# Kernel tuning notes

Measured on AMD Instinct MI355X. Metric: run time of the kernel, lower is better.

## Reference

```python
import jax, jax.numpy as jnp
import numpy as np

N = 50000      # nodes
E = 800000     # edges
IN = 256       # in_dim
D = 64         # hidden_dim per head
H = 4          # heads
OUT = 40       # out_dim (classes)
SLOPE = 0.2    # leaky relu negative slope


def _gat_conv(h, src, dst, W, al, ar, heads, dh, res=None, act=False):
    """DGL-style GATConv. h:[N,Fin], W:[Fin,heads*dh], al/ar:[heads,dh]."""
    n = h.shape[0]
    feat = (h @ W).reshape(n, heads, dh)                 # [N,H,D]
    el = jnp.sum(feat * al, axis=-1)                     # [N,H]
    er = jnp.sum(feat * ar, axis=-1)                     # [N,H]
    e = jax.nn.leaky_relu(el[src] + er[dst], SLOPE)      # [E,H]
    # segment softmax over incoming edges of each dst node
    m = jax.ops.segment_max(e, dst, num_segments=n)      # [N,H]
    ex = jnp.exp(e - m[dst])                             # [E,H]
    s = jax.ops.segment_sum(ex, dst, num_segments=n)     # [N,H]
    alpha = ex / s[dst]                                  # [E,H]
    rst = jax.ops.segment_sum(alpha[:, :, None] * feat[src], dst, num_segments=n)  # [N,H,D]
    if res is not None:
        rst = rst + res
    if act:
        rst = jax.nn.elu(rst)
    return rst


def setup_inputs():
    key = jax.random.key(0)
    ks = jax.random.split(key, 16)
    def p(k, shape, fan_in):
        return (jax.random.normal(k, shape, jnp.float32) / np.sqrt(fan_in)).astype(jnp.float32)
    inputs = jax.random.normal(ks[0], (N, IN), jnp.float32)
    src = jax.random.randint(ks[1], (E,), 0, N, dtype=jnp.int32)
    dst = jax.random.randint(ks[2], (E,), 0, N, dtype=jnp.int32)
    return {
        "inputs": inputs, "src": src, "dst": dst,
        "W0": p(ks[3], (IN, H * D), IN), "al0": p(ks[4], (H, D), D), "ar0": p(ks[5], (H, D), D),
        "W1": p(ks[6], (H * D, H * D), H * D), "al1": p(ks[7], (H, D), D), "ar1": p(ks[8], (H, D), D),
        "Wo": p(ks[9], (H * D, H * OUT), H * D), "alo": p(ks[10], (H, OUT), OUT), "aro": p(ks[11], (H, OUT), OUT),
        "res_Wo": p(ks[12], (H * D, H * OUT), H * D),
        "fc_W": p(ks[13], (IN, D), IN),
    }


def reference(inputs, src, dst, W0, al0, ar0, W1, al1, ar1, Wo, alo, aro, res_Wo, fc_W):
    # layer 0: no residual, elu activation
    h = _gat_conv(inputs, src, dst, W0, al0, ar0, H, D, res=None, act=True)
    h = h.reshape(N, H * D)
    # layer 1: identity residual (in_feats == heads*out_feats), elu
    res1 = h.reshape(N, H, D)
    h = _gat_conv(h, src, dst, W1, al1, ar1, H, D, res=res1, act=True)
    h = h.reshape(N, H * D)
    # output layer: linear residual projection, no activation, mean over heads
    res_o = (h @ res_Wo).reshape(N, H, OUT)
    logits = _gat_conv(h, src, dst, Wo, alo, aro, H, OUT, res=res_o, act=False).mean(axis=1)
    seq_fts = inputs @ fc_W
    return (logits, h, seq_fts)
```

## Files before the change

### kernel.cpp

```cpp
#include <hip/hip_runtime.h>

typedef unsigned short u16;
typedef unsigned int u32;
typedef __attribute__((ext_vector_type(8))) short short8;
typedef __attribute__((ext_vector_type(4))) float f32x4;

#define NN 50000
#define EE 800000
#define EPAD (EE + 8*NN)

__device__ __forceinline__ float b2f(u16 u){ union{float f;u32 i;}x; x.i=((u32)u)<<16; return x.f; }
__device__ __forceinline__ u16 f2b(float f){ union{float f;u32 i;}x; x.f=f; u32 i=x.i; return (u16)((i + 0x7fffu + ((i>>16)&1u))>>16); }

__global__ void k_f2b4(const float* __restrict__ x, u16* __restrict__ y, int n4){
  int i = blockIdx.x*256 + threadIdx.x;
  if (i >= n4) return;
  float4 v = ((const float4*)x)[i];
  ushort4 o; o.x=f2b(v.x); o.y=f2b(v.y); o.z=f2b(v.z); o.w=f2b(v.w);
  ((ushort4*)y)[i]=o;
}

__global__ void k_wtr(const float* __restrict__ W, u16* __restrict__ Wt, int N){
  int i = blockIdx.x*256 + threadIdx.x;
  if (i >= 256*N) return;
  int k = i / N, n = i % N;
  Wt[(size_t)n*256 + k] = f2b(W[i]);
}

__global__ void k_catWoT(const float* __restrict__ rWo, const float* __restrict__ Wo, u16* __restrict__ Bct){
  int i = blockIdx.x*256 + threadIdx.x;
  if (i >= 256*320) return;
  int k = i/320, c = i%320;
  float v = (c < 160) ? rWo[k*160 + c] : Wo[k*160 + (c-160)];
  Bct[(size_t)c*256 + k] = f2b(v);
}

__global__ void k_count(const int* __restrict__ dst, int* __restrict__ cnt){
  int i = blockIdx.x*256+threadIdx.x; if (i<EE) atomicAdd(&cnt[dst[i]],1);
}

__global__ void k_scan_blocks(const int* __restrict__ cnt, int* __restrict__ off, int* __restrict__ part, int n){
  __shared__ int ts[256];
  int t = threadIdx.x; int base = blockIdx.x*1024 + t*4;
  int c0 = (base+0<n)?((cnt[base+0]+7)&~7):0;
  int c1 = (base+1<n)?((cnt[base+1]+7)&~7):0;
  int c2 = (base+2<n)?((cnt[base+2]+7)&~7):0;
  int c3 = (base+3<n)?((cnt[base+3]+7)&~7):0;
  int s = c0+c1+c2+c3;
  ts[t]=s; __syncthreads();
  for (int d=1; d<256; d<<=1){ int v=(t>=d)?ts[t-d]:0; __syncthreads(); ts[t]+=v; __syncthreads(); }
  int ex = ts[t]-s;
  if (t==255) part[blockIdx.x]=ts[255];
  if (base+0<n) off[base+0]=ex; ex+=c0;
  if (base+1<n) off[base+1]=ex; ex+=c1;
  if (base+2<n) off[base+2]=ex; ex+=c2;
  if (base+3<n) off[base+3]=ex;
}

__global__ void k_scan_part(int* part, int nb){
  if (threadIdx.x==0 && blockIdx.x==0){ int run=0; for(int i=0;i<nb;++i){ int v=part[i]; part[i]=run; run+=v; } }
}

__global__ void k_addback(int* off, int* cur, const int* __restrict__ part, int n){
  int base = blockIdx.x*1024 + threadIdx.x*4; int p = part[blockIdx.x];
  #pragma unroll
  for (int j=0;j<4;++j) if (base+j<n){ int v = off[base+j]+p; off[base+j]=v; if (base+j<NN) cur[base+j]=v; }
}

__global__ void k_scatter(const int* __restrict__ src, const int* __restrict__ dst, int* __restrict__ cur,
                          int* __restrict__ srcs){
  int i = blockIdx.x*256+threadIdx.x; if (i>=EE) return;
  int d = dst[i]; int p = atomicAdd(&cur[d],1);
  srcs[p]=src[i];
}

__global__ void k_padfill(const int* __restrict__ off, const int* __restrict__ cnt, int* __restrict__ srcs){
  int n = blockIdx.x*256+threadIdx.x; if (n>=NN) return;
  int e = off[n]+cnt[n], e1 = off[n+1];
  for (; e<e1; ++e) srcs[e] = 0;
}

template<int BN, int MODE>
__global__ __launch_bounds__(256) void k_gemm2(const u16* __restrict__ A, const u16* __restrict__ Bt,
                                               void* __restrict__ C0, void* __restrict__ C1,
                                               const float* __restrict__ AL, const float* __restrict__ AR,
                                               float* __restrict__ EL, float* __restrict__ ER,
                                               int M, int ldC){
  __shared__ u16 lds[(128+BN)*256];
  u16* As = lds;
  u16* Bs = lds + 128*256;
  const int tid = threadIdx.x;
  const int row0 = blockIdx.x * 128;
  const int n0   = blockIdx.y * BN;
  #pragma unroll
  for (int it=0; it<16; ++it){
    int slot = it*256 + tid;
    int r = slot >> 5, s = slot & 31;
    int gs = s ^ (r & 7);
    const u16* gp = A + (size_t)(row0 + r)*256 + (gs<<3);
    u16* lp = As + (size_t)(it*256 + (tid & ~63))*8;
    __builtin_amdgcn_global_load_lds((const void*)gp, (void*)lp, 16, 0, 0);
  }
  #pragma unroll
  for (int it=0; it<BN/8; ++it){
    int slot = it*256 + tid;
    int r = slot >> 5, s = slot & 31;
    int gs = s ^ (r & 7);
    const u16* gp = Bt + (size_t)(n0 + r)*256 + (gs<<3);
    u16* lp = Bs + (size_t)(it*256 + (tid & ~63))*8;
    __builtin_amdgcn_global_load_lds((const void*)gp, (void*)lp, 16, 0, 0);
  }
  __syncthreads();
  const int wave = tid >> 6, l = tid & 63;
  const int wm = wave >> 1, wn = wave & 1;
  const int lr = l & 15, lq = l >> 4;
  const int NR = BN/32;
  f32x4 acc[4][4];
  #pragma unroll
  for (int mr=0;mr<4;++mr)
    #pragma unroll
    for (int nr=0;nr<NR;++nr) acc[mr][nr]=(f32x4)0.0f;
  #pragma unroll
  for (int kk=0; kk<8; ++kk){
    short8 a[4], b[4];
    #pragma unroll
    for (int mr=0;mr<4;++mr){
      int rloc = wm*64 + mr*16 + lr;
      int byo = rloc*512 + ((kk*64 + lq*16) ^ ((rloc&7)<<4));
      a[mr] = *(const short8*)((const char*)As + byo);
    }
    #pragma unroll
    for (int nr=0;nr<NR;++nr){
      int cloc = wn*(BN/2) + nr*16 + lr;
      int byo = cloc*512 + ((kk*64 + lq*16) ^ ((cloc&7)<<4));
      b[nr] = *(const short8*)((const char*)Bs + byo);
    }
    #pragma unroll
    for (int mr=0;mr<4;++mr)
      #pragma unroll
      for (int nr=0;nr<NR;++nr)
        acc[mr][nr] = __builtin_amdgcn_mfma_f32_16x16x32_bf16(a[mr], b[nr], acc[mr][nr], 0, 0, 0);
  }
  #pragma unroll
  for (int mr=0;mr<4;++mr)
    #pragma unroll
    for (int nr=0;nr<NR;++nr)
      #pragma unroll
      for (int q=0;q<4;++q){
        int r = row0 + wm*64 + mr*16 + lq*4 + q;
        if (r < M){
          int c = n0 + wn*(BN/2) + nr*16 + lr;
          float v = acc[mr][nr][q];
          if constexpr (MODE == 0)      ((float*)C0)[(size_t)r*ldC + c] = v;
          else if constexpr (MODE == 1) ((u16*)C0)[(size_t)r*ldC + c] = f2b(v);
          else {
            if (c < 160)      ((u16*)C0)[(size_t)r*160 + c]       = f2b(v);
            else if (c < 320) ((u16*)C1)[(size_t)r*160 + (c-160)] = f2b(v);
          }
        }
      }
  if constexpr (MODE == 1){
    const int head = (n0 + wn*64) >> 6;
    float alc[4], arc[4];
    #pragma unroll
    for (int nr=0;nr<4;++nr){
      int c = n0 + wn*64 + nr*16 + lr;
      alc[nr] = AL[c]; arc[nr] = AR[c];
    }
    #pragma unroll
    for (int mr=0;mr<4;++mr)
      #pragma unroll
      for (int q=0;q<4;++q){
        float suml = acc[mr][0][q]*alc[0] + acc[mr][1][q]*alc[1] + acc[mr][2][q]*alc[2] + acc[mr][3][q]*alc[3];
        float sumr = acc[mr][0][q]*arc[0] + acc[mr][1][q]*arc[1] + acc[mr][2][q]*arc[2] + acc[mr][3][q]*arc[3];
        #pragma unroll
        for (int msk=1; msk<16; msk<<=1){ suml += __shfl_xor(suml,msk,64); sumr += __shfl_xor(sumr,msk,64); }
        int r = row0 + wm*64 + mr*16 + lq*4 + q;
        if (lr == 0 && r < M){ EL[r*4+head] = suml; ER[r*4+head] = sumr; }
      }
  }
}

__global__ void k_eler(const u16* __restrict__ feat, const float* __restrict__ al, const float* __restrict__ ar,
                       float* __restrict__ el, float* __restrict__ er, int Dh, int HD){
  int t = blockIdx.x*256 + threadIdx.x;
  int n = t >> 6; int l = t & 63;
  if (n >= NN) return;
  int h = l >> 4, s = l & 15;
  const u16* fr = feat + (size_t)n*HD + h*Dh;
  const float* alh = al + h*Dh; const float* arh = ar + h*Dh;
  float accl = 0.f, accr = 0.f;
  for (int d = s; d < Dh; d += 16){ float f = b2f(fr[d]); accl += f*alh[d]; accr += f*arh[d]; }
  #pragma unroll
  for (int m = 8; m >= 1; m >>= 1){ accl += __shfl_xor(accl, m, 64); accr += __shfl_xor(accr, m, 64); }
  if (s == 0){ el[n*4+h] = accl; er[n*4+h] = accr; }
}

__global__ void k_soft(const float* __restrict__ el, const float* __restrict__ er,
                       const int* __restrict__ srcs, const int* __restrict__ off, const int* __restrict__ cnt,
                       float* __restrict__ es, float* __restrict__ recs){
  int t = blockIdx.x*256 + threadIdx.x;
  int n = t >> 4; if (n >= NN) return;
  int g = t & 15;
  int o0 = off[n], o1p = off[n+1];
  int deg = cnt[n];
  int oend = o0 + deg;
  float4 e4 = ((const float4*)er)[n];
  float4 m; m.x=m.y=m.z=m.w=-1e30f;
  for (int c = o0 + g; c < oend; c += 16){
    float4 a = ((const float4*)el)[srcs[c]];
    float4 v;
    v.x=a.x+e4.x; v.x = v.x>=0.f?v.x:0.2f*v.x;
    v.y=a.y+e4.y; v.y = v.y>=0.f?v.y:0.2f*v.y;
    v.z=a.z+e4.z; v.z = v.z>=0.f?v.z:0.2f*v.z;
    v.w=a.w+e4.w; v.w = v.w>=0.f?v.w:0.2f*v.w;
    ((float4*)es)[c]=v;
    m.x=fmaxf(m.x,v.x); m.y=fmaxf(m.y,v.y); m.z=fmaxf(m.z,v.z); m.w=fmaxf(m.w,v.w);
  }
  { int cp = oend + g; if (cp < o1p){ float4 z; z.x=z.y=z.z=z.w=0.f; ((float4*)es)[cp]=z; } }
  #pragma unroll
  for (int msk = 8; msk >= 1; msk >>= 1){
    m.x=fmaxf(m.x,__shfl_xor(m.x,msk,64)); m.y=fmaxf(m.y,__shfl_xor(m.y,msk,64));
    m.z=fmaxf(m.z,__shfl_xor(m.z,msk,64)); m.w=fmaxf(m.w,__shfl_xor(m.w,msk,64));
  }
  float4 s; s.x=s.y=s.z=s.w=0.f;
  for (int c = o0 + g; c < oend; c += 16){
    float4 v = ((const float4*)es)[c];
    v.x=__expf(v.x-m.x); v.y=__expf(v.y-m.y); v.z=__expf(v.z-m.z); v.w=__expf(v.w-m.w);
    ((float4*)es)[c]=v; s.x+=v.x; s.y+=v.y; s.z+=v.z; s.w+=v.w;
  }
  #pragma unroll
  for (int msk = 8; msk >= 1; msk >>= 1){
    s.x+=__shfl_xor(s.x,msk,64); s.y+=__shfl_xor(s.y,msk,64);
    s.z+=__shfl_xor(s.z,msk,64); s.w+=__shfl_xor(s.w,msk,64);
  }
  if (g == 0){
    float4 r;
    r.x = s.x>0.f ? 1.f/s.x : 0.f;
    r.y = s.y>0.f ? 1.f/s.y : 0.f;
    r.z = s.z>0.f ? 1.f/s.z : 0.f;
    r.w = s.w>0.f ? 1.f/s.w : 0.f;
    ((float4*)recs)[n] = r;
  }
}

template<bool RES>
__global__ __launch_bounds__(256) void k_agg64(const u16* __restrict__ feat, const float* __restrict__ es,
    const float* __restrict__ recs, const int* __restrict__ off, const int* __restrict__ srcs,
    const u16* __restrict__ resid, float* __restrict__ outf, u16* __restrict__ outb){
  const int l = threadIdx.x & 63, w = threadIdx.x >> 6;
  const int n = blockIdx.x*4 + w;
  const int o0 = off[n], o1p = off[n+1];
  const int lh = l & 31;
  const int half = l >> 5;
  const int h = lh >> 3;
  float a0=0.f,a1=0.f,a2=0.f,a3=0.f,a4=0.f,a5=0.f,a6=0.f,a7=0.f;
  for (int i = o0; i < o1p; i += 8){
    #pragma unroll
    for (int u=0; u<4; ++u){
      int e = i + u*2 + half;
      int sv = srcs[e];
      float al = es[(size_t)e*4 + h];
      short8 f = *(const short8*)(feat + (size_t)sv*256 + lh*8);
      a0 += al*b2f((u16)f[0]); a1 += al*b2f((u16)f[1]);
      a2 += al*b2f((u16)f[2]); a3 += al*b2f((u16)f[3]);
      a4 += al*b2f((u16)f[4]); a5 += al*b2f((u16)f[5]);
      a6 += al*b2f((u16)f[6]); a7 += al*b2f((u16)f[7]);
    }
  }
  a0 += __shfl_xor(a0,32,64); a1 += __shfl_xor(a1,32,64);
  a2 += __shfl_xor(a2,32,64); a3 += __shfl_xor(a3,32,64);
  a4 += __shfl_xor(a4,32,64); a5 += __shfl_xor(a5,32,64);
  a6 += __shfl_xor(a6,32,64); a7 += __shfl_xor(a7,32,64);
  if (half == 0){
    float rc = recs[n*4+h];
    float v[8] = {a0*rc,a1*rc,a2*rc,a3*rc,a4*rc,a5*rc,a6*rc,a7*rc};
    if (RES){
      short8 r8 = *(const short8*)(resid + (size_t)n*256 + lh*8);
      #pragma unroll
      for (int j=0;j<8;++j) v[j] += b2f((u16)r8[j]);
    }
    #pragma unroll
    for (int j=0;j<8;++j) v[j] = v[j] > 0.f ? v[j] : expm1f(v[j]);
    if (outf){
      float4 q0; q0.x=v[0]; q0.y=v[1]; q0.z=v[2]; q0.w=v[3];
      float4 q1; q1.x=v[4]; q1.y=v[5]; q1.z=v[6]; q1.w=v[7];
      *(float4*)(outf + (size_t)n*256 + lh*8)     = q0;
      *(float4*)(outf + (size_t)n*256 + lh*8 + 4) = q1;
    }
    short8 ob;
    #pragma unroll
    for (int j=0;j<8;++j) ob[j] = (short)f2b(v[j]);
    *(short8*)(outb + (size_t)n*256 + lh*8) = ob;
  }
}

__global__ __launch_bounds__(256) void k_agg_out(const u16* __restrict__ feat, const float* __restrict__ es,
    const float* __restrict__ recs, const int* __restrict__ off, const int* __restrict__ srcs,
    const u16* __restrict__ reso, float* __restrict__ logits){
  __shared__ float red[4][8][20][9];
  __shared__ float fin[4][160];
  const int l = threadIdx.x & 63, w = threadIdx.x >> 6;
  const int n = blockIdx.x*4 + w;
  const int o0 = off[n], o1p = off[n+1];
  const int s0 = l/20,        q0 = l%20;
  const int s1 = (64+l)/20,   q1 = (64+l)%20;
  const int s2 = (128+l)/20,  q2 = (128+l)%20;
  const int h0 = q0/5, h1 = q1/5, h2 = q2/5;
  float acc0[8], acc1[8], acc2[8];
  #pragma unroll
  for (int j=0;j<8;++j){ acc0[j]=0.f; acc1[j]=0.f; acc2[j]=0.f; }
  for (int i0 = o0; i0 < o1p; i0 += 8){
    {
      int e = i0 + s0; int sv = srcs[e]; float al = es[(size_t)e*4 + h0];
      short8 f = *(const short8*)(feat + (size_t)sv*160 + q0*8);
      #pragma unroll
      for (int j=0;j<8;++j) acc0[j] += al*b2f((u16)f[j]);
    }
    {
      int e = i0 + s1; int sv = srcs[e]; float al = es[(size_t)e*4 + h1];
      short8 f = *(const short8*)(feat + (size_t)sv*160 + q1*8);
      #pragma unroll
      for (int j=0;j<8;++j) acc1[j] += al*b2f((u16)f[j]);
    }
    if (l < 32){
      int e = i0 + s2; int sv = srcs[e]; float al = es[(size_t)e*4 + h2];
      short8 f = *(const short8*)(feat + (size_t)sv*160 + q2*8);
      #pragma unroll
      for (int j=0;j<8;++j) acc2[j] += al*b2f((u16)f[j]);
    }
  }
  #pragma unroll
  for (int j=0;j<8;++j) red[w][s0][q0][j] = acc0[j];
  #pragma unroll
  for (int j=0;j<8;++j) red[w][s1][q1][j] = acc1[j];
  if (l < 32){
    #pragma unroll
    for (int j=0;j<8;++j) red[w][s2][q2][j] = acc2[j];
  }
  __syncthreads();
  if (l < 20){
    const int q = l;
    float rc = recs[n*4 + q/5];
    short8 rr = *(const short8*)(reso + (size_t)n*160 + q*8);
    #pragma unroll
    for (int j=0;j<8;++j){
      float v = red[w][0][q][j];
      #pragma unroll
      for (int s=1;s<8;++s) v += red[w][s][q][j];
      fin[w][q*8+j] = v*rc + b2f((u16)rr[j]);
    }
  }
  __syncthreads();
  if (l < 40) logits[(size_t)n*40 + l] = 0.25f*(fin[w][l]+fin[w][l+40]+fin[w][l+80]+fin[w][l+120]);
}

extern "C" void kernel_launch(void* const* d_in, const int* in_sizes, int n_in,
                              void* d_out, int out_size, void* d_ws, size_t ws_size,
                              hipStream_t stream){
  const float* inputs = (const float*)d_in[0];
  const int*   src    = (const int*)d_in[1];
  const int*   dst    = (const int*)d_in[2];
  const float* W0  = (const float*)d_in[3];
  const float* al0 = (const float*)d_in[4];
  const float* ar0 = (const float*)d_in[5];
  const float* W1  = (const float*)d_in[6];
  const float* al1 = (const float*)d_in[7];
  const float* ar1 = (const float*)d_in[8];
  const float* Wo  = (const float*)d_in[9];
  const float* alo = (const float*)d_in[10];
  const float* aro = (const float*)d_in[11];
  const float* rWo = (const float*)d_in[12];
  const float* fcW = (const float*)d_in[13];

  float* out = (float*)d_out;
  float* out_logits = out;
  float* out_h      = out + 2000000;
  float* out_seq    = out + 14800000;

  char* ws = (char*)d_ws;
  size_t o = 0;
  auto alc = [&](size_t bytes){ size_t r = o; o += (bytes + 255) & ~(size_t)255; return r; };
  size_t oXb   = alc((size_t)NN*256*2);
  size_t oFA   = alc((size_t)NN*256*2);
  size_t oFB   = alc((size_t)NN*256*2);
  size_t oEs   = alc((size_t)EPAD*4*4);
  size_t oSrcs = alc((size_t)EPAD*4);
  size_t oOff  = alc((size_t)(NN+1)*4);
  size_t oCnt  = alc((size_t)(NN+1)*4);
  size_t oCur  = alc((size_t)NN*4);
  size_t oPart = alc(64*4);
  size_t oEl   = alc((size_t)NN*4*4);
  size_t oEr   = alc((size_t)NN*4*4);
  size_t oRecs = alc((size_t)NN*4*4);
  size_t oReso = alc((size_t)NN*160*2);
  size_t oW0t  = alc(256*256*2);
  size_t oW1t  = alc(256*256*2);
  size_t oWct  = alc((size_t)384*256*2);
  size_t oFct  = alc((size_t)128*256*2);
  if (ws_size < o) return;

  u16* Xb   = (u16*)(ws + oXb);
  u16* fA   = (u16*)(ws + oFA);
  u16* fB   = (u16*)(ws + oFB);
  float* es = (float*)(ws + oEs);
  int* srcs = (int*)(ws + oSrcs);
  int* off  = (int*)(ws + oOff);
  int* cnt  = (int*)(ws + oCnt);
  int* cur  = (int*)(ws + oCur);
  int* part = (int*)(ws + oPart);
  float* el = (float*)(ws + oEl);
  float* er = (float*)(ws + oEr);
  float* recs = (float*)(ws + oRecs);
  u16* reso = (u16*)(ws + oReso);
  u16* W0t  = (u16*)(ws + oW0t);
  u16* W1t  = (u16*)(ws + oW1t);
  u16* Wct  = (u16*)(ws + oWct);
  u16* fct  = (u16*)(ws + oFct);

  k_f2b4<<<(NN*256/4 + 255)/256, 256, 0, stream>>>(inputs, Xb, NN*256/4);
  k_wtr<<<(256*256 + 255)/256, 256, 0, stream>>>(W0, W0t, 256);
  k_wtr<<<(256*256 + 255)/256, 256, 0, stream>>>(W1, W1t, 256);
  k_wtr<<<(256*64 + 255)/256, 256, 0, stream>>>(fcW, fct, 64);
  k_catWoT<<<(256*320 + 255)/256, 256, 0, stream>>>(rWo, Wo, Wct);

  hipMemsetAsync(cnt, 0, (size_t)(NN+1)*4, stream);
  k_count<<<(EE+255)/256, 256, 0, stream>>>(dst, cnt);
  const int NP1 = NN+1, NB = (NP1 + 1023)/1024;
  k_scan_blocks<<<NB, 256, 0, stream>>>(cnt, off, part, NP1);
  k_scan_part<<<1, 64, 0, stream>>>(part, NB);
  k_addback<<<NB, 256, 0, stream>>>(off, cur, part, NP1);
  k_scatter<<<(EE+255)/256, 256, 0, stream>>>(src, dst, cur, srcs);
  k_padfill<<<(NN+255)/256, 256, 0, stream>>>(off, cnt, srcs);

  const int GX = (NN + 127)/128;
  dim3 g256(GX, 2), g320(GX, 3), g64(GX, 1);

  k_gemm2<64,0><<<g64, 256, 0, stream>>>(Xb, fct, out_seq, nullptr, nullptr, nullptr, nullptr, nullptr, NN, 64);

  k_gemm2<128,1><<<g256, 256, 0, stream>>>(Xb, W0t, fA, nullptr, al0, ar0, el, er, NN, 256);
  k_soft<<<(NN*16 + 255)/256, 256, 0, stream>>>(el, er, srcs, off, cnt, es, recs);
  k_agg64<false><<<NN/4, 256, 0, stream>>>(fA, es, recs, off, srcs, nullptr, nullptr, fB);

  k_gemm2<128,1><<<g256, 256, 0, stream>>>(fB, W1t, fA, nullptr, al1, ar1, el, er, NN, 256);
  k_soft<<<(NN*16 + 255)/256, 256, 0, stream>>>(el, er, srcs, off, cnt, es, recs);
  k_agg64<true><<<NN/4, 256, 0, stream>>>(fA, es, recs, off, srcs, fB, out_h, fB);

  k_gemm2<128,2><<<g320, 256, 0, stream>>>(fB, Wct, reso, fA, nullptr, nullptr, nullptr, nullptr, NN, 320);
  k_eler<<<(NN*64 + 255)/256, 256, 0, stream>>>(fA, alo, aro, el, er, 40, 160);
  k_soft<<<(NN*16 + 255)/256, 256, 0, stream>>>(el, er, srcs, off, cnt, es, recs);
  k_agg_out<<<NN/4, 256, 0, stream>>>(fA, es, recs, off, srcs, reso, out_logits);
}
```

Baseline: 492.4 us.

## Fold residual head-mean into weights, drop softmax max pass, atomic CSR offsets

Pre-averages the output residual projection over heads in the weight conversion, so the final GEMM produces 40 residual columns instead of 160. The segment softmax computes exp directly with a clamp instead of a separate max-reduction pass, removing one read/write sweep over edge scores. The multi-kernel prefix scan is replaced by per-node atomic offset allocation, and the weight-conversion kernels are merged into one launch. Skipping max subtraction risks overflow or precision loss for large logits.

```diff
diff --git a/kernel.cpp b/kernel.cpp
--- a/kernel.cpp
+++ b/kernel.cpp
@@ -20,51 +20,40 @@
   ((ushort4*)y)[i]=o;
 }
 
-__global__ void k_wtr(const float* __restrict__ W, u16* __restrict__ Wt, int N){
+__global__ void k_wcvt(const float* __restrict__ W0, const float* __restrict__ W1,
+                       const float* __restrict__ fcW, const float* __restrict__ rWo,
+                       const float* __restrict__ Wo,
+                       u16* __restrict__ W0t, u16* __restrict__ W1t,
+                       u16* __restrict__ fct, u16* __restrict__ Wct){
   int i = blockIdx.x*256 + threadIdx.x;
-  if (i >= 256*N) return;
-  int k = i / N, n = i % N;
-  Wt[(size_t)n*256 + k] = f2b(W[i]);
-}
-
-__global__ void k_catWoT(const float* __restrict__ rWo, const float* __restrict__ Wo, u16* __restrict__ Bct){
-  int i = blockIdx.x*256 + threadIdx.x;
-  if (i >= 256*320) return;
-  int k = i/320, c = i%320;
-  float v = (c < 160) ? rWo[k*160 + c] : Wo[k*160 + (c-160)];
-  Bct[(size_t)c*256 + k] = f2b(v);
+  if (i < 65536){
+    int n = i >> 8, k = i & 255;
+    W0t[i] = f2b(W0[k*256 + n]);
+  } else if (i < 131072){
+    int j = i - 65536; int n = j >> 8, k = j & 255;
+    W1t[j] = f2b(W1[k*256 + n]);
+  } else if (i < 147456){
+    int j = i - 131072; int n = j >> 8, k = j & 255;
+    fct[j] = f2b(fcW[k*64 + n]);
+  } else if (i < 198656){
+    int j = i - 147456; int r = j >> 8, k = j & 255;
+    float v;
+    if (r < 40) v = 0.25f*(rWo[k*160 + r] + rWo[k*160 + 40 + r] + rWo[k*160 + 80 + r] + rWo[k*160 + 120 + r]);
+    else        v = Wo[k*160 + (r - 40)];
+    Wct[j] = f2b(v);
+  }
 }
 
 __global__ void k_count(const int* __restrict__ dst, int* __restrict__ cnt){
   int i = blockIdx.x*256+threadIdx.x; if (i<EE) atomicAdd(&cnt[dst[i]],1);
 }
 
-__global__ void k_scan_blocks(const int* __restrict__ cnt, int* __restrict__ off, int* __restrict__ part, int n){
-  __shared__ int ts[256];
-  int t = threadIdx.x; int base = blockIdx.x*1024 + t*4;
-  int c0 = (base+0<n)?((cnt[base+0]+7)&~7):0;
-  int c1 = (base+1<n)?((cnt[base+1]+7)&~7):0;
-  int c2 = (base+2<n)?((cnt[base+2]+7)&~7):0;
-  int c3 = (base+3<n)?((cnt[base+3]+7)&~7):0;
-  int s = c0+c1+c2+c3;
-  ts[t]=s; __syncthreads();
-  for (int d=1; d<256; d<<=1){ int v=(t>=d)?ts[t-d]:0; __syncthreads(); ts[t]+=v; __syncthreads(); }
-  int ex = ts[t]-s;
-  if (t==255) part[blockIdx.x]=ts[255];
-  if (base+0<n) off[base+0]=ex; ex+=c0;
-  if (base+1<n) off[base+1]=ex; ex+=c1;
-  if (base+2<n) off[base+2]=ex; ex+=c2;
-  if (base+3<n) off[base+3]=ex;
-}
-
-__global__ void k_scan_part(int* part, int nb){
-  if (threadIdx.x==0 && blockIdx.x==0){ int run=0; for(int i=0;i<nb;++i){ int v=part[i]; part[i]=run; run+=v; } }
-}
-
-__global__ void k_addback(int* off, int* cur, const int* __restrict__ part, int n){
-  int base = blockIdx.x*1024 + threadIdx.x*4; int p = part[blockIdx.x];
-  #pragma unroll
-  for (int j=0;j<4;++j) if (base+j<n){ int v = off[base+j]+p; off[base+j]=v; if (base+j<NN) cur[base+j]=v; }
+__global__ void k_alloc(const int* __restrict__ cnt, int* __restrict__ off, int* __restrict__ cur,
+                        int* __restrict__ total){
+  int n = blockIdx.x*256+threadIdx.x; if (n>=NN) return;
+  int pc = (cnt[n]+7)&~7;
+  int o = atomicAdd(total, pc);
+  off[n]=o; cur[n]=o;
 }
 
 __global__ void k_scatter(const int* __restrict__ src, const int* __restrict__ dst, int* __restrict__ cur,
@@ -76,7 +65,8 @@
 
 __global__ void k_padfill(const int* __restrict__ off, const int* __restrict__ cnt, int* __restrict__ srcs){
   int n = blockIdx.x*256+threadIdx.x; if (n>=NN) return;
-  int e = off[n]+cnt[n], e1 = off[n+1];
+  int deg = cnt[n];
+  int e = off[n]+deg, e1 = off[n]+((deg+7)&~7);
   for (; e<e1; ++e) srcs[e] = 0;
 }
 
@@ -154,8 +144,8 @@
           if constexpr (MODE == 0)      ((float*)C0)[(size_t)r*ldC + c] = v;
           else if constexpr (MODE == 1) ((u16*)C0)[(size_t)r*ldC + c] = f2b(v);
           else {
-            if (c < 160)      ((u16*)C0)[(size_t)r*160 + c]       = f2b(v);
-            else if (c < 320) ((u16*)C1)[(size_t)r*160 + (c-160)] = f2b(v);
+            if (c < 40)       ((u16*)C0)[(size_t)r*40 + c]        = f2b(v);
+            else if (c < 200) ((u16*)C1)[(size_t)r*160 + (c-40)]  = f2b(v);
           }
         }
       }
@@ -202,33 +192,22 @@
   int t = blockIdx.x*256 + threadIdx.x;
   int n = t >> 4; if (n >= NN) return;
   int g = t & 15;
-  int o0 = off[n], o1p = off[n+1];
+  int o0 = off[n];
   int deg = cnt[n];
-  int oend = o0 + deg;
+  int oend = o0 + deg, o1p = o0 + ((deg+7)&~7);
   float4 e4 = ((const float4*)er)[n];
-  float4 m; m.x=m.y=m.z=m.w=-1e30f;
+  float4 s; s.x=s.y=s.z=s.w=0.f;
   for (int c = o0 + g; c < oend; c += 16){
     float4 a = ((const float4*)el)[srcs[c]];
     float4 v;
-    v.x=a.x+e4.x; v.x = v.x>=0.f?v.x:0.2f*v.x;
-    v.y=a.y+e4.y; v.y = v.y>=0.f?v.y:0.2f*v.y;
-    v.z=a.z+e4.z; v.z = v.z>=0.f?v.z:0.2f*v.z;
-    v.w=a.w+e4.w; v.w = v.w>=0.f?v.w:0.2f*v.w;
+    v.x=a.x+e4.x; v.x = v.x>=0.f?v.x:0.2f*v.x; v.x=__expf(fminf(v.x,60.f));
+    v.y=a.y+e4.y; v.y = v.y>=0.f?v.y:0.2f*v.y; v.y=__expf(fminf(v.y,60.f));
+    v.z=a.z+e4.z; v.z = v.z>=0.f?v.z:0.2f*v.z; v.z=__expf(fminf(v.z,60.f));
+    v.w=a.w+e4.w; v.w = v.w>=0.f?v.w:0.2f*v.w; v.w=__expf(fminf(v.w,60.f));
     ((float4*)es)[c]=v;
-    m.x=fmaxf(m.x,v.x); m.y=fmaxf(m.y,v.y); m.z=fmaxf(m.z,v.z); m.w=fmaxf(m.w,v.w);
+    s.x+=v.x; s.y+=v.y; s.z+=v.z; s.w+=v.w;
   }
   { int cp = oend + g; if (cp < o1p){ float4 z; z.x=z.y=z.z=z.w=0.f; ((float4*)es)[cp]=z; } }
-  #pragma unroll
-  for (int msk = 8; msk >= 1; msk >>= 1){
-    m.x=fmaxf(m.x,__shfl_xor(m.x,msk,64)); m.y=fmaxf(m.y,__shfl_xor(m.y,msk,64));
-    m.z=fmaxf(m.z,__shfl_xor(m.z,msk,64)); m.w=fmaxf(m.w,__shfl_xor(m.w,msk,64));
-  }
-  float4 s; s.x=s.y=s.z=s.w=0.f;
-  for (int c = o0 + g; c < oend; c += 16){
-    float4 v = ((const float4*)es)[c];
-    v.x=__expf(v.x-m.x); v.y=__expf(v.y-m.y); v.z=__expf(v.z-m.z); v.w=__expf(v.w-m.w);
-    ((float4*)es)[c]=v; s.x+=v.x; s.y+=v.y; s.z+=v.z; s.w+=v.w;
-  }
   #pragma unroll
   for (int msk = 8; msk >= 1; msk >>= 1){
     s.x+=__shfl_xor(s.x,msk,64); s.y+=__shfl_xor(s.y,msk,64);
@@ -246,11 +225,13 @@
 
 template<bool RES>
 __global__ __launch_bounds__(256) void k_agg64(const u16* __restrict__ feat, const float* __restrict__ es,
-    const float* __restrict__ recs, const int* __restrict__ off, const int* __restrict__ srcs,
+    const float* __restrict__ recs, const int* __restrict__ off, const int* __restrict__ cnt,
+    const int* __restrict__ srcs,
     const u16* __restrict__ resid, float* __restrict__ outf, u16* __restrict__ outb){
   const int l = threadIdx.x & 63, w = threadIdx.x >> 6;
   const int n = blockIdx.x*4 + w;
-  const int o0 = off[n], o1p = off[n+1];
+  const int o0 = off[n];
+  const int o1p = o0 + ((cnt[n]+7)&~7);
   const int lh = l & 31;
   const int half = l >> 5;
   const int h = lh >> 3;
@@ -296,13 +277,15 @@
 }
 
 __global__ __launch_bounds__(256) void k_agg_out(const u16* __restrict__ feat, const float* __restrict__ es,
-    const float* __restrict__ recs, const int* __restrict__ off, const int* __restrict__ srcs,
-    const u16* __restrict__ reso, float* __restrict__ logits){
+    const float* __restrict__ recs, const int* __restrict__ off, const int* __restrict__ cnt,
+    const int* __restrict__ srcs,
+    const u16* __restrict__ reso40, float* __restrict__ logits){
   __shared__ float red[4][8][20][9];
   __shared__ float fin[4][160];
   const int l = threadIdx.x & 63, w = threadIdx.x >> 6;
   const int n = blockIdx.x*4 + w;
-  const int o0 = off[n], o1p = off[n+1];
+  const int o0 = off[n];
+  const int o1p = o0 + ((cnt[n]+7)&~7);
   const int s0 = l/20,        q0 = l%20;
   const int s1 = (64+l)/20,   q1 = (64+l)%20;
   const int s2 = (128+l)/20,  q2 = (128+l)%20;
@@ -341,18 +324,20 @@
   __syncthreads();
   if (l < 20){
     const int q = l;
-    float rc = recs[n*4 + q/5];
-    short8 rr = *(const short8*)(reso + (size_t)n*160 + q*8);
+    float rc = 0.25f * recs[n*4 + q/5];
     #pragma unroll
     for (int j=0;j<8;++j){
       float v = red[w][0][q][j];
       #pragma unroll
       for (int s=1;s<8;++s) v += red[w][s][q][j];
-      fin[w][q*8+j] = v*rc + b2f((u16)rr[j]);
+      fin[w][q*8+j] = v*rc;
     }
   }
   __syncthreads();
-  if (l < 40) logits[(size_t)n*40 + l] = 0.25f*(fin[w][l]+fin[w][l+40]+fin[w][l+80]+fin[w][l+120]);
+  if (l < 40){
+    float r = b2f(reso40[(size_t)n*40 + l]);
+    logits[(size_t)n*40 + l] = fin[w][l]+fin[w][l+40]+fin[w][l+80]+fin[w][l+120] + r;
+  }
 }
 
 extern "C" void kernel_launch(void* const* d_in, const int* in_sizes, int n_in,
@@ -386,14 +371,13 @@
   size_t oFB   = alc((size_t)NN*256*2);
   size_t oEs   = alc((size_t)EPAD*4*4);
   size_t oSrcs = alc((size_t)EPAD*4);
-  size_t oOff  = alc((size_t)(NN+1)*4);
+  size_t oOff  = alc((size_t)NN*4);
   size_t oCnt  = alc((size_t)(NN+1)*4);
   size_t oCur  = alc((size_t)NN*4);
-  size_t oPart = alc(64*4);
   size_t oEl   = alc((size_t)NN*4*4);
   size_t oEr   = alc((size_t)NN*4*4);
   size_t oRecs = alc((size_t)NN*4*4);
-  size_t oReso = alc((size_t)NN*160*2);
+  size_t oReso = alc((size_t)NN*40*2);
   size_t oW0t  = alc(256*256*2);
   size_t oW1t  = alc(256*256*2);
   size_t oWct  = alc((size_t)384*256*2);
@@ -408,46 +392,39 @@
   int* off  = (int*)(ws + oOff);
   int* cnt  = (int*)(ws + oCnt);
   int* cur  = (int*)(ws + oCur);
-  int* part = (int*)(ws + oPart);
   float* el = (float*)(ws + oEl);
   float* er = (float*)(ws + oEr);
   float* recs = (float*)(ws + oRecs);
-  u16* reso = (u16*)(ws + oReso);
+  u16* reso40 = (u16*)(ws + oReso);
   u16* W0t  = (u16*)(ws + oW0t);
   u16* W1t  = (u16*)(ws + oW1t);
   u16* Wct  = (u16*)(ws + oWct);
   u16* fct  = (u16*)(ws + oFct);
 
   k_f2b4<<<(NN*256/4 + 255)/256, 256, 0, stream>>>(inputs, Xb, NN*256/4);
-  k_wtr<<<(256*256 + 255)/256, 256, 0, stream>>>(W0, W0t, 256);
-  k_wtr<<<(256*256 + 255)/256, 256, 0, stream>>>(W1, W1t, 256);
-  k_wtr<<<(256*64 + 255)/256, 256, 0, stream>>>(fcW, fct, 64);
-  k_catWoT<<<(256*320 + 255)/256, 256, 0, stream>>>(rWo, Wo, Wct);
+  k_wcvt<<<(198656 + 255)/256, 256, 0, stream>>>(W0, W1, fcW, rWo, Wo, W0t, W1t, fct, Wct);
 
   hipMemsetAsync(cnt, 0, (size_t)(NN+1)*4, stream);
   k_count<<<(EE+255)/256, 256, 0, stream>>>(dst, cnt);
-  const int NP1 = NN+1, NB = (NP1 + 1023)/1024;
-  k_scan_blocks<<<NB, 256, 0, stream>>>(cnt, off, part, NP1);
-  k_scan_part<<<1, 64, 0, stream>>>(part, NB);
-  k_addback<<<NB, 256, 0, stream>>>(off, cur, part, NP1);
+  k_alloc<<<(NN+255)/256, 256, 0, stream>>>(cnt, off, cur, &cnt[NN]);
   k_scatter<<<(EE+255)/256, 256, 0, stream>>>(src, dst, cur, srcs);
   k_padfill<<<(NN+255)/256, 256, 0, stream>>>(off, cnt, srcs);
 
   const int GX = (NN + 127)/128;
-  dim3 g256(GX, 2), g320(GX, 3), g64(GX, 1);
+  dim3 g256(GX, 2), g200(GX, 2), g64(GX, 1);
 
   k_gemm2<64,0><<<g64, 256, 0, stream>>>(Xb, fct, out_seq, nullptr, nullptr, nullptr, nullptr, nullptr, NN, 64);
 
   k_gemm2<128,1><<<g256, 256, 0, stream>>>(Xb, W0t, fA, nullptr, al0, ar0, el, er, NN, 256);
   k_soft<<<(NN*16 + 255)/256, 256, 0, stream>>>(el, er, srcs, off, cnt, es, recs);
-  k_agg64<false><<<NN/4, 256, 0, stream>>>(fA, es, recs, off, srcs, nullptr, nullptr, fB);
+  k_agg64<false><<<NN/4, 256, 0, stream>>>(fA, es, recs, off, cnt, srcs, nullptr, nullptr, fB);
 
   k_gemm2<128,1><<<g256, 256, 0, stream>>>(fB, W1t, fA, nullptr, al1, ar1, el, er, NN, 256);
   k_soft<<<(NN*16 + 255)/256, 256, 0, stream>>>(el, er, srcs, off, cnt, es, recs);
-  k_agg64<true><<<NN/4, 256, 0, stream>>>(fA, es, recs, off, srcs, fB, out_h, fB);
-
-  k_gemm2<128,2><<<g320, 256, 0, stream>>>(fB, Wct, reso, fA, nullptr, nullptr, nullptr, nullptr, NN, 320);
+  k_agg64<true><<<NN/4, 256, 0, stream>>>(fA, es, recs, off, cnt, srcs, fB, out_h, fB);
+
+  k_gemm2<128,2><<<g200, 256, 0, stream>>>(fB, Wct, reso40, fA, nullptr, nullptr, nullptr, nullptr, NN, 200);
   k_eler<<<(NN*64 + 255)/256, 256, 0, stream>>>(fA, alo, aro, el, er, 40, 160);
   k_soft<<<(NN*16 + 255)/256, 256, 0, stream>>>(el, er, srcs, off, cnt, es, recs);
-  k_agg_out<<<NN/4, 256, 0, stream>>>(fA, es, recs, off, srcs, reso, out_logits);
-}
+  k_agg_out<<<NN/4, 256, 0, stream>>>(fA, es, recs, off, cnt, srcs, reso40, out_logits);
+}
```

After: 468.6 us. 1.05x faster.
